# Optimization experiments

Hardware: AMD Instinct MI355X
Metric: run time of the kernel (lower is better)

## Reference

```python
import jax, jax.numpy as jnp
import numpy as np

INPUT_DIM = 256
HIDDEN_DIM = 512
BATCH = 64
SEQ = 512


def setup_inputs() -> dict:
    key = jax.random.key(0)
    k1, k2, k3, k4, k5 = jax.random.split(key, 5)
    s = 1.0 / np.sqrt(HIDDEN_DIM)
    x = jax.random.normal(k1, (BATCH, SEQ, INPUT_DIM), dtype=jnp.float32)
    # PyTorch GRU param layout: [3*H, in] with gate order (r, z, n)
    W_ih = jax.random.uniform(k2, (3 * HIDDEN_DIM, INPUT_DIM), minval=-s, maxval=s, dtype=jnp.float32)
    W_hh = jax.random.uniform(k3, (3 * HIDDEN_DIM, HIDDEN_DIM), minval=-s, maxval=s, dtype=jnp.float32)
    b_ih = jax.random.uniform(k4, (3 * HIDDEN_DIM,), minval=-s, maxval=s, dtype=jnp.float32)
    b_hh = jax.random.uniform(k5, (3 * HIDDEN_DIM,), minval=-s, maxval=s, dtype=jnp.float32)
    return {"x": x, "W_ih": W_ih, "W_hh": W_hh, "b_ih": b_ih, "b_hh": b_hh}


def _gru_last(x, W_ih, W_hh, b_ih, b_hh):
    B, T, _ = x.shape
    H = W_hh.shape[1]
    # Precompute input projections for all timesteps: [B, T, 3H]
    x_proj = jnp.einsum('bti,gi->btg', x, W_ih) + b_ih
    x_proj = jnp.swapaxes(x_proj, 0, 1)  # [T, B, 3H] for scan

    def step(h, xp):
        h_proj = h @ W_hh.T + b_hh  # [B, 3H]
        xr, xz, xn = jnp.split(xp, 3, axis=-1)
        hr, hz, hn = jnp.split(h_proj, 3, axis=-1)
        r = jax.nn.sigmoid(xr + hr)
        z = jax.nn.sigmoid(xz + hz)
        n = jnp.tanh(xn + r * hn)
        h_new = (1.0 - z) * n + z * h
        return h_new, None

    h0 = jnp.zeros((B, H), dtype=x.dtype)
    h_last, _ = jax.lax.scan(step, h0, x_proj)
    return h_last  # equals output[:, -1, :] for unidirectional single-layer GRU


def reference(x, W_ih, W_hh, b_ih, b_hh):
    return _gru_last(x, W_ih, W_hh, b_ih, b_hh)
```

## Files before the change

kernel.cpp:

```cpp
#include <hip/hip_runtime.h>
#include <hip/hip_bf16.h>


#define NB 64
#define NT 512
#define NI 256
#define NH 512

typedef __attribute__((ext_vector_type(8))) short bf16x8;
typedef __attribute__((ext_vector_type(4))) float f32x4;
typedef __attribute__((ext_vector_type(4))) int i32x4;

static __device__ __forceinline__ short f2b(float f) {
  unsigned u = __builtin_bit_cast(unsigned, f);
  unsigned r = (u + 0x7fffu + ((u >> 16) & 1u)) >> 16;
  return (short)r;
}
static __device__ __forceinline__ float sigm(float x) {
  return 1.0f / (1.0f + __expf(-x));
}
static __device__ __forceinline__ float tanh_f(float x) {
  return 1.0f - 2.0f / (__expf(2.0f * x) + 1.0f);
}

__global__ __launch_bounds__(256, 1)
void gru_persistent(const float* __restrict__ x,
                    const float* __restrict__ Wih,
                    const float* __restrict__ Whh,
                    const float* __restrict__ bih,
                    const float* __restrict__ bhh,
                    float* __restrict__ out,
                    unsigned char* __restrict__ ws) {
  const int wg   = blockIdx.x;
  const int tid  = threadIdx.x;
  const int wave = tid >> 6;
  const int lane = tid & 63;
  const int c    = lane & 15;
  const int q    = lane >> 4;

  int* slots = (int*)ws;
  int* tags  = (int*)(ws + 8192);
  unsigned short* hb0 = (unsigned short*)(ws + 16384);
  unsigned short* hb1 = (unsigned short*)(ws + 16384 + 65536);
  unsigned short* xb  = (unsigned short*)(ws + 16384 + 2 * 65536);

  __shared__ unsigned short trans[4][16][8];

  {
    const float4* x4 = (const float4*)x;
    const int total4 = NB * NT * NI / 4;
    const int nthr = NB * 256;
    for (int i = wg * 256 + tid; i < total4; i += nthr) {
      float4 v = x4[i];
      ushort4 o;
      o.x = (unsigned short)f2b(v.x);
      o.y = (unsigned short)f2b(v.y);
      o.z = (unsigned short)f2b(v.z);
      o.w = (unsigned short)f2b(v.w);
      ((ushort4*)xb)[i] = o;
    }
    ((unsigned int*)hb0)[wg * 256 + tid] = 0u;
    if (wg == 0) tags[tid] = 0;
  }

  bf16x8 wh[2][16];
  bf16x8 wi[2][8];
#pragma unroll
  for (int nt = 0; nt < 2; nt++) {
    int nl = nt * 16 + c;
    bool valid = nl < 24;
    int gate = nl >> 3;
    int jj = nl & 7;
    int grow = valid ? (gate * NH + wg * 8 + jj) : 0;
#pragma unroll
    for (int kk = 0; kk < 16; kk++) {
      const float* p = Whh + (size_t)grow * NH + kk * 32 + q * 8;
      bf16x8 f;
#pragma unroll
      for (int e = 0; e < 8; e++) f[e] = valid ? f2b(p[e]) : (short)0;
      wh[nt][kk] = f;
    }
#pragma unroll
    for (int kk = 0; kk < 8; kk++) {
      const float* p = Wih + (size_t)grow * NI + kk * 32 + q * 8;
      bf16x8 f;
#pragma unroll
      for (int e = 0; e < 8; e++) f[e] = valid ? f2b(p[e]) : (short)0;
      wi[nt][kk] = f;
    }
  }

  const int jcol = wg * 8 + (c & 7);
  const float bri = bih[jcol],          brh = bhh[jcol];
  const float bzi = bih[NH + jcol],     bzh = bhh[NH + jcol];
  const float bni = bih[2 * NH + jcol], bnh = bhh[2 * NH + jcol];

  float hold[4] = {0.f, 0.f, 0.f, 0.f};

  __syncthreads();
  if (tid == 0)
    __hip_atomic_store(&slots[wg * 32], 1, __ATOMIC_RELEASE,
                       __HIP_MEMORY_SCOPE_AGENT);
  if (wave == 0) {
    while (__hip_atomic_load(&slots[lane * 32], __ATOMIC_RELAXED,
                             __HIP_MEMORY_SCOPE_AGENT) < 1)
      __builtin_amdgcn_s_sleep(1);
  }
  __syncthreads();
  __threadfence();

  const int b0 = wave * 16 + c;
  int* mytags = tags + wave * 64;
  const int* tagp = mytags + lane;

  for (int t = 0; t < NT; t++) {
    const unsigned short* hcur = (t & 1) ? hb1 : hb0;
    unsigned short* hnext      = (t & 1) ? hb0 : hb1;

    f32x4 aX0 = {0.f, 0.f, 0.f, 0.f}, aX1 = {0.f, 0.f, 0.f, 0.f};
    f32x4 aH0 = {0.f, 0.f, 0.f, 0.f}, aH1 = {0.f, 0.f, 0.f, 0.f};

    const bf16x8* xr = (const bf16x8*)(xb + ((size_t)b0 * NT + t) * NI);

#pragma unroll
    for (int kk = 0; kk < 8; kk++) {
      bf16x8 a = xr[kk * 4 + q];
      aX0 = __builtin_amdgcn_mfma_f32_16x16x32_bf16(a, wi[0][kk], aX0, 0, 0, 0);
      aX1 = __builtin_amdgcn_mfma_f32_16x16x32_bf16(a, wi[1][kk], aX1, 0, 0, 0);
    }

    if (t > 0) {
      const int need = t + 1;
      while (true) {
        int v;
        asm volatile("global_load_dword %0, %1, off sc1"
                     : "=v"(v) : "v"(tagp));
        asm volatile("s_waitcnt vmcnt(0)" : "+v"(v)::"memory");
        if (__all(v >= need)) break;
      }
    }

    i32x4 hv[16];
    {
      const char* hb = (const char*)hcur;
#pragma unroll
      for (int kk = 0; kk < 16; kk++) {
        const void* ap = hb + (size_t)(((kk * 4 + q) * 64 + b0) << 4);
        asm volatile("global_load_dwordx4 %0, %1, off sc1"
                     : "=v"(hv[kk]) : "v"(ap));
      }
      asm volatile("s_waitcnt vmcnt(0)"
                   : "+v"(hv[0]), "+v"(hv[1]), "+v"(hv[2]), "+v"(hv[3]),
                     "+v"(hv[4]), "+v"(hv[5]), "+v"(hv[6]), "+v"(hv[7]),
                     "+v"(hv[8]), "+v"(hv[9]), "+v"(hv[10]), "+v"(hv[11]),
                     "+v"(hv[12]), "+v"(hv[13]), "+v"(hv[14]), "+v"(hv[15])
                   ::"memory");
    }

#pragma unroll
    for (int kk = 0; kk < 16; kk++) {
      bf16x8 a = __builtin_bit_cast(bf16x8, hv[kk]);
      aH0 = __builtin_amdgcn_mfma_f32_16x16x32_bf16(a, wh[0][kk], aH0, 0, 0, 0);
      aH1 = __builtin_amdgcn_mfma_f32_16x16x32_bf16(a, wh[1][kk], aH1, 0, 0, 0);
    }

#pragma unroll
    for (int r = 0; r < 4; r++) {
      float xz = __shfl_xor(aX0[r], 8, 64);
      float hz = __shfl_xor(aH0[r], 8, 64);
      float rr = sigm(aX0[r] + bri + aH0[r] + brh);
      float zz = sigm(xz + bzi + hz + bzh);
      float nn = tanh_f(aX1[r] + bni + rr * (aH1[r] + bnh));
      float hv2 = (1.0f - zz) * nn + zz * hold[r];
      hold[r] = hv2;
      if (c < 8) trans[wave][q * 4 + r][c] = (unsigned short)f2b(hv2);
    }

    if (t < NT - 1) {
      asm volatile("s_waitcnt lgkmcnt(0)" ::: "memory");
      if (lane < 16) {
        int b = wave * 16 + lane;
        const unsigned long long* tp =
            (const unsigned long long*)&trans[wave][lane][0];
        unsigned long long v0 = tp[0], v1 = tp[1];
        unsigned long long* dst =
            (unsigned long long*)(hnext + ((size_t)wg * 64 + b) * 8);
        __hip_atomic_store(dst, v0, __ATOMIC_RELAXED, __HIP_MEMORY_SCOPE_AGENT);
        __hip_atomic_store(dst + 1, v1, __ATOMIC_RELAXED,
                           __HIP_MEMORY_SCOPE_AGENT);
      }
      asm volatile("s_waitcnt vmcnt(0)" ::: "memory");
      if (lane == 0)
        __hip_atomic_store(&mytags[wg], t + 2, __ATOMIC_RELAXED,
                           __HIP_MEMORY_SCOPE_AGENT);
    }
  }

  if (c < 8) {
#pragma unroll
    for (int r = 0; r < 4; r++) {
      int b = wave * 16 + q * 4 + r;
      out[(size_t)b * NH + wg * 8 + c] = hold[r];
    }
  }
}

extern "C" void kernel_launch(void* const* d_in, const int* in_sizes, int n_in,
                              void* d_out, int out_size, void* d_ws, size_t ws_size,
                              hipStream_t stream) {
  const float* x   = (const float*)d_in[0];
  const float* Wih = (const float*)d_in[1];
  const float* Whh = (const float*)d_in[2];
  const float* bih = (const float*)d_in[3];
  const float* bhh = (const float*)d_in[4];
  float* out = (float*)d_out;
  hipLaunchKernelGGL(gru_persistent, dim3(NB), dim3(256), 0, stream,
                     x, Wih, Whh, bih, bhh, out, (unsigned char*)d_ws);
}
```

Baseline: 1.834 ms.

## Spread workgroups across XCDs and use non-coherent fast path with runtime coherence test

Launches 512 blocks so every eighth block (one per XCD stride) becomes a persistent worker while all blocks share the x-to-bf16 conversion. At startup the workers run a timestamp-based barrier and a store/invalidate/load coherence test. If it passes, the recurrent loop switches to plain stores and loads with buffer_inv instead of sc1 system-coherent accesses, which cuts the latency of each per-step h exchange. This depends on the assumption that co-located workers share a coherent L2. A timeout and a demotion flag fall back to the old sc1 path.

```diff
diff --git a/kernel.cpp b/kernel.cpp
--- a/kernel.cpp
+++ b/kernel.cpp
@@ -7,6 +7,17 @@
 #define NI 256
 #define NH 512
 
+#define OFF_FLAGS   0u
+#define OFF_TSB1    32768u
+#define OFF_TSB2    36864u
+#define OFF_TSB3    40960u
+#define OFF_DEMOTE  45056u
+#define OFF_TESTA   49152u
+#define OFF_TAGS    57344u
+#define OFF_HB0     65536u
+#define OFF_HB1     131072u
+#define OFF_XB      262144u
+
 typedef __attribute__((ext_vector_type(8))) short bf16x8;
 typedef __attribute__((ext_vector_type(4))) float f32x4;
 typedef __attribute__((ext_vector_type(4))) int i32x4;
@@ -23,72 +34,57 @@
   return 1.0f - 2.0f / (__expf(2.0f * x) + 1.0f);
 }
 
-__global__ __launch_bounds__(256, 1)
-void gru_persistent(const float* __restrict__ x,
-                    const float* __restrict__ Wih,
-                    const float* __restrict__ Whh,
-                    const float* __restrict__ bih,
-                    const float* __restrict__ bhh,
-                    float* __restrict__ out,
-                    unsigned char* __restrict__ ws) {
-  const int wg   = blockIdx.x;
-  const int tid  = threadIdx.x;
+static __device__ __forceinline__ void tsbar(unsigned char* base, int rank,
+                                             int tid, int wave, int lane,
+                                             unsigned long long t0) {
+  __syncthreads();
+  if (tid == 0)
+    __hip_atomic_store((unsigned long long*)(base + (size_t)rank * 64),
+                       __builtin_amdgcn_s_memrealtime(), __ATOMIC_RELEASE,
+                       __HIP_MEMORY_SCOPE_AGENT);
+  if (wave == 0) {
+    while (__hip_atomic_load(
+               (const unsigned long long*)(base + (size_t)lane * 64),
+               __ATOMIC_RELAXED, __HIP_MEMORY_SCOPE_AGENT) < t0)
+      __builtin_amdgcn_s_sleep(1);
+  }
+  __syncthreads();
+  __threadfence();
+}
+
+#define LOAD_ALL(FLAG)                                                        \
+  do {                                                                        \
+    const char* hbase_ = (const char*)hcur;                                   \
+    _Pragma("unroll") for (int kk2 = 0; kk2 < 16; kk2++) {                    \
+      const void* ap_ = hbase_ + (size_t)(((kk2 * 4 + q) * 64 + b0) << 4);    \
+      asm volatile("global_load_dwordx4 %0, %1, off " FLAG                    \
+                   : "=v"(hv[kk2]) : "v"(ap_));                               \
+    }                                                                         \
+  } while (0)
+
+#define WAIT_ALL()                                                            \
+  asm volatile("s_waitcnt vmcnt(0)"                                           \
+               : "+v"(hv[0]), "+v"(hv[1]), "+v"(hv[2]), "+v"(hv[3]),          \
+                 "+v"(hv[4]), "+v"(hv[5]), "+v"(hv[6]), "+v"(hv[7]),          \
+                 "+v"(hv[8]), "+v"(hv[9]), "+v"(hv[10]), "+v"(hv[11]),        \
+                 "+v"(hv[12]), "+v"(hv[13]), "+v"(hv[14]), "+v"(hv[15])       \
+               ::"memory")
+
+template <bool FAST>
+static __device__ __forceinline__ void worker_body(
+    int wg, int tid, const float* __restrict__ bih,
+    const float* __restrict__ bhh, float* __restrict__ out,
+    unsigned char* __restrict__ ws, const bf16x8 wh[2][16],
+    const bf16x8 wi[2][8], unsigned short (*trans)[16][8]) {
   const int wave = tid >> 6;
   const int lane = tid & 63;
   const int c    = lane & 15;
   const int q    = lane >> 4;
 
-  int* slots = (int*)ws;
-  int* tags  = (int*)(ws + 8192);
-  unsigned short* hb0 = (unsigned short*)(ws + 16384);
-  unsigned short* hb1 = (unsigned short*)(ws + 16384 + 65536);
-  unsigned short* xb  = (unsigned short*)(ws + 16384 + 2 * 65536);
-
-  __shared__ unsigned short trans[4][16][8];
-
-  {
-    const float4* x4 = (const float4*)x;
-    const int total4 = NB * NT * NI / 4;
-    const int nthr = NB * 256;
-    for (int i = wg * 256 + tid; i < total4; i += nthr) {
-      float4 v = x4[i];
-      ushort4 o;
-      o.x = (unsigned short)f2b(v.x);
-      o.y = (unsigned short)f2b(v.y);
-      o.z = (unsigned short)f2b(v.z);
-      o.w = (unsigned short)f2b(v.w);
-      ((ushort4*)xb)[i] = o;
-    }
-    ((unsigned int*)hb0)[wg * 256 + tid] = 0u;
-    if (wg == 0) tags[tid] = 0;
-  }
-
-  bf16x8 wh[2][16];
-  bf16x8 wi[2][8];
-#pragma unroll
-  for (int nt = 0; nt < 2; nt++) {
-    int nl = nt * 16 + c;
-    bool valid = nl < 24;
-    int gate = nl >> 3;
-    int jj = nl & 7;
-    int grow = valid ? (gate * NH + wg * 8 + jj) : 0;
-#pragma unroll
-    for (int kk = 0; kk < 16; kk++) {
-      const float* p = Whh + (size_t)grow * NH + kk * 32 + q * 8;
-      bf16x8 f;
-#pragma unroll
-      for (int e = 0; e < 8; e++) f[e] = valid ? f2b(p[e]) : (short)0;
-      wh[nt][kk] = f;
-    }
-#pragma unroll
-    for (int kk = 0; kk < 8; kk++) {
-      const float* p = Wih + (size_t)grow * NI + kk * 32 + q * 8;
-      bf16x8 f;
-#pragma unroll
-      for (int e = 0; e < 8; e++) f[e] = valid ? f2b(p[e]) : (short)0;
-      wi[nt][kk] = f;
-    }
-  }
+  int* tags = (int*)(ws + OFF_TAGS);
+  unsigned short* hb0 = (unsigned short*)(ws + OFF_HB0);
+  unsigned short* hb1 = (unsigned short*)(ws + OFF_HB1);
+  const unsigned short* xb = (const unsigned short*)(ws + OFF_XB);
 
   const int jcol = wg * 8 + (c & 7);
   const float bri = bih[jcol],          brh = bhh[jcol];
@@ -97,18 +93,6 @@
 
   float hold[4] = {0.f, 0.f, 0.f, 0.f};
 
-  __syncthreads();
-  if (tid == 0)
-    __hip_atomic_store(&slots[wg * 32], 1, __ATOMIC_RELEASE,
-                       __HIP_MEMORY_SCOPE_AGENT);
-  if (wave == 0) {
-    while (__hip_atomic_load(&slots[lane * 32], __ATOMIC_RELAXED,
-                             __HIP_MEMORY_SCOPE_AGENT) < 1)
-      __builtin_amdgcn_s_sleep(1);
-  }
-  __syncthreads();
-  __threadfence();
-
   const int b0 = wave * 16 + c;
   int* mytags = tags + wave * 64;
   const int* tagp = mytags + lane;
@@ -117,51 +101,50 @@
     const unsigned short* hcur = (t & 1) ? hb1 : hb0;
     unsigned short* hnext      = (t & 1) ? hb0 : hb1;
 
-    f32x4 aX0 = {0.f, 0.f, 0.f, 0.f}, aX1 = {0.f, 0.f, 0.f, 0.f};
-    f32x4 aH0 = {0.f, 0.f, 0.f, 0.f}, aH1 = {0.f, 0.f, 0.f, 0.f};
+    f32x4 aX0 = {0.f,0.f,0.f,0.f}, aX1 = {0.f,0.f,0.f,0.f};
+    f32x4 aH0 = {0.f,0.f,0.f,0.f}, aH1 = {0.f,0.f,0.f,0.f};
 
     const bf16x8* xr = (const bf16x8*)(xb + ((size_t)b0 * NT + t) * NI);
 
 #pragma unroll
     for (int kk = 0; kk < 8; kk++) {
       bf16x8 a = xr[kk * 4 + q];
-      aX0 = __builtin_amdgcn_mfma_f32_16x16x32_bf16(a, wi[0][kk], aX0, 0, 0, 0);
-      aX1 = __builtin_amdgcn_mfma_f32_16x16x32_bf16(a, wi[1][kk], aX1, 0, 0, 0);
+      aX0 = __builtin_amdgcn_mfma_f32_16x16x32_bf16(a, wi[0][kk], aX0, 0,0,0);
+      aX1 = __builtin_amdgcn_mfma_f32_16x16x32_bf16(a, wi[1][kk], aX1, 0,0,0);
     }
 
     if (t > 0) {
       const int need = t + 1;
-      while (true) {
-        int v;
-        asm volatile("global_load_dword %0, %1, off sc1"
-                     : "=v"(v) : "v"(tagp));
-        asm volatile("s_waitcnt vmcnt(0)" : "+v"(v)::"memory");
-        if (__all(v >= need)) break;
+      if (FAST) {
+        for (;;) {
+          asm volatile("buffer_inv sc0" ::: "memory");
+          int v;
+          asm volatile("global_load_dword %0, %1, off" : "=v"(v) : "v"(tagp));
+          asm volatile("s_waitcnt vmcnt(0)" : "+v"(v)::"memory");
+          if (__all(v >= need)) break;
+        }
+      } else {
+        for (;;) {
+          int v;
+          asm volatile("global_load_dword %0, %1, off sc1"
+                       : "=v"(v) : "v"(tagp));
+          asm volatile("s_waitcnt vmcnt(0)" : "+v"(v)::"memory");
+          if (__all(v >= need)) break;
+        }
       }
+    } else if (FAST) {
+      asm volatile("buffer_inv sc0" ::: "memory");
     }
 
     i32x4 hv[16];
-    {
-      const char* hb = (const char*)hcur;
-#pragma unroll
-      for (int kk = 0; kk < 16; kk++) {
-        const void* ap = hb + (size_t)(((kk * 4 + q) * 64 + b0) << 4);
-        asm volatile("global_load_dwordx4 %0, %1, off sc1"
-                     : "=v"(hv[kk]) : "v"(ap));
-      }
-      asm volatile("s_waitcnt vmcnt(0)"
-                   : "+v"(hv[0]), "+v"(hv[1]), "+v"(hv[2]), "+v"(hv[3]),
-                     "+v"(hv[4]), "+v"(hv[5]), "+v"(hv[6]), "+v"(hv[7]),
-                     "+v"(hv[8]), "+v"(hv[9]), "+v"(hv[10]), "+v"(hv[11]),
-                     "+v"(hv[12]), "+v"(hv[13]), "+v"(hv[14]), "+v"(hv[15])
-                   ::"memory");
-    }
+    if (FAST) LOAD_ALL(""); else LOAD_ALL("sc1");
+    WAIT_ALL();
 
 #pragma unroll
     for (int kk = 0; kk < 16; kk++) {
       bf16x8 a = __builtin_bit_cast(bf16x8, hv[kk]);
-      aH0 = __builtin_amdgcn_mfma_f32_16x16x32_bf16(a, wh[0][kk], aH0, 0, 0, 0);
-      aH1 = __builtin_amdgcn_mfma_f32_16x16x32_bf16(a, wh[1][kk], aH1, 0, 0, 0);
+      aH0 = __builtin_amdgcn_mfma_f32_16x16x32_bf16(a, wh[0][kk], aH0, 0,0,0);
+      aH1 = __builtin_amdgcn_mfma_f32_16x16x32_bf16(a, wh[1][kk], aH1, 0,0,0);
     }
 
 #pragma unroll
@@ -180,19 +163,26 @@
       asm volatile("s_waitcnt lgkmcnt(0)" ::: "memory");
       if (lane < 16) {
         int b = wave * 16 + lane;
-        const unsigned long long* tp =
-            (const unsigned long long*)&trans[wave][lane][0];
-        unsigned long long v0 = tp[0], v1 = tp[1];
-        unsigned long long* dst =
-            (unsigned long long*)(hnext + ((size_t)wg * 64 + b) * 8);
-        __hip_atomic_store(dst, v0, __ATOMIC_RELAXED, __HIP_MEMORY_SCOPE_AGENT);
-        __hip_atomic_store(dst + 1, v1, __ATOMIC_RELAXED,
-                           __HIP_MEMORY_SCOPE_AGENT);
+        i32x4 pk = *(const i32x4*)&trans[wave][lane][0];
+        void* dst = (char*)hnext + ((size_t)(wg * 64 + b) << 4);
+        if (FAST)
+          asm volatile("global_store_dwordx4 %0, %1, off"
+                       :: "v"(dst), "v"(pk) : "memory");
+        else
+          asm volatile("global_store_dwordx4 %0, %1, off sc1"
+                       :: "v"(dst), "v"(pk) : "memory");
       }
       asm volatile("s_waitcnt vmcnt(0)" ::: "memory");
-      if (lane == 0)
-        __hip_atomic_store(&mytags[wg], t + 2, __ATOMIC_RELAXED,
-                           __HIP_MEMORY_SCOPE_AGENT);
+      if (lane == 0) {
+        int* tp = &mytags[wg];
+        int tv = t + 2;
+        if (FAST)
+          asm volatile("global_store_dword %0, %1, off"
+                       :: "v"(tp), "v"(tv) : "memory");
+        else
+          __hip_atomic_store(tp, tv, __ATOMIC_RELAXED,
+                             __HIP_MEMORY_SCOPE_AGENT);
+      }
     }
   }
 
@@ -203,6 +193,146 @@
       out[(size_t)b * NH + wg * 8 + c] = hold[r];
     }
   }
+}
+
+__global__ __launch_bounds__(256, 2)
+void gru_persistent(const float* __restrict__ x,
+                    const float* __restrict__ Wih,
+                    const float* __restrict__ Whh,
+                    const float* __restrict__ bih,
+                    const float* __restrict__ bhh,
+                    float* __restrict__ out,
+                    unsigned char* __restrict__ ws) {
+  const int bid  = blockIdx.x;
+  const int tid  = threadIdx.x;
+  const int wave = tid >> 6;
+  const int lane = tid & 63;
+  const int c    = lane & 15;
+  const int q    = lane >> 4;
+
+  const unsigned long long t0 = __builtin_amdgcn_s_memrealtime();
+
+  unsigned long long* flags = (unsigned long long*)(ws + OFF_FLAGS);
+  int* tags = (int*)(ws + OFF_TAGS);
+  unsigned* hb0d = (unsigned*)(ws + OFF_HB0);
+  unsigned short* xb = (unsigned short*)(ws + OFF_XB);
+
+  __shared__ __align__(16) unsigned short trans[4][16][8];
+  __shared__ int s_bad;
+
+  const bool is_worker = (bid & 7) == 0;
+  const int rank = bid >> 3;
+
+  {
+    const float4* x4 = (const float4*)x;
+    const int total4 = NB * NT * NI / 4;
+    const int nthr = 512 * 256;
+    for (int i = bid * 256 + tid; i < total4; i += nthr) {
+      float4 v = x4[i];
+      ushort4 o;
+      o.x = (unsigned short)f2b(v.x);
+      o.y = (unsigned short)f2b(v.y);
+      o.z = (unsigned short)f2b(v.z);
+      o.w = (unsigned short)f2b(v.w);
+      ((ushort4*)xb)[i] = o;
+    }
+    if (is_worker) hb0d[rank * 256 + tid] = 0u;
+    if (bid == 0) tags[tid] = 0;
+  }
+
+  __syncthreads();
+  if (tid == 0)
+    __hip_atomic_store(&flags[bid * 8], __builtin_amdgcn_s_memrealtime(),
+                       __ATOMIC_RELEASE, __HIP_MEMORY_SCOPE_AGENT);
+  if (!is_worker) return;
+
+  bf16x8 wh[2][16];
+  bf16x8 wi[2][8];
+#pragma unroll
+  for (int nt = 0; nt < 2; nt++) {
+    int nl = nt * 16 + c;
+    bool valid = nl < 24;
+    int gate = nl >> 3;
+    int jj = nl & 7;
+    int grow = valid ? (gate * NH + rank * 8 + jj) : 0;
+#pragma unroll
+    for (int kk = 0; kk < 16; kk++) {
+      const float* p = Whh + (size_t)grow * NH + kk * 32 + q * 8;
+      bf16x8 f;
+#pragma unroll
+      for (int e = 0; e < 8; e++) f[e] = valid ? f2b(p[e]) : (short)0;
+      wh[nt][kk] = f;
+    }
+#pragma unroll
+    for (int kk = 0; kk < 8; kk++) {
+      const float* p = Wih + (size_t)grow * NI + kk * 32 + q * 8;
+      bf16x8 f;
+#pragma unroll
+      for (int e = 0; e < 8; e++) f[e] = valid ? f2b(p[e]) : (short)0;
+      wi[nt][kk] = f;
+    }
+  }
+
+  if (wave == 0) {
+#pragma unroll
+    for (int j = 0; j < 8; j++) {
+      const unsigned long long dl = t0 + 200000ull;
+      while (__hip_atomic_load(&flags[(lane * 8 + j) * 8], __ATOMIC_RELAXED,
+                               __HIP_MEMORY_SCOPE_AGENT) < t0) {
+        if (__builtin_amdgcn_s_memrealtime() > dl) break;
+        __builtin_amdgcn_s_sleep(1);
+      }
+    }
+  }
+  __syncthreads();
+  __threadfence();
+
+  if (tid == 0) s_bad = 0;
+  if (wave == 0) {
+    int v;
+    const void* p = ws + OFF_TESTA + (size_t)lane * 64;
+    asm volatile("global_load_dword %0, %1, off" : "=v"(v) : "v"(p));
+    asm volatile("s_waitcnt vmcnt(0)" : "+v"(v)::"memory");
+  }
+  tsbar(ws + OFF_TSB1, rank, tid, wave, lane, t0);
+  const unsigned ep = (unsigned)__hip_atomic_load(
+      (const unsigned long long*)(ws + OFF_TSB1), __ATOMIC_RELAXED,
+      __HIP_MEMORY_SCOPE_AGENT);
+  if (tid == 0) {
+    unsigned mg = (ep ^ 0x5EEDBEEFu) + (unsigned)rank * 2654435761u;
+    void* p = ws + OFF_TESTA + (size_t)rank * 64;
+    asm volatile("global_store_dword %0, %1, off" :: "v"(p), "v"(mg)
+                 : "memory");
+    asm volatile("s_waitcnt vmcnt(0)" ::: "memory");
+  }
+  tsbar(ws + OFF_TSB2, rank, tid, wave, lane, t0);
+  {
+    int bad = 0;
+    if (wave == 0) {
+      asm volatile("buffer_inv sc0" ::: "memory");
+      int v;
+      const void* p = ws + OFF_TESTA + (size_t)lane * 64;
+      asm volatile("global_load_dword %0, %1, off" : "=v"(v) : "v"(p));
+      asm volatile("s_waitcnt vmcnt(0)" : "+v"(v)::"memory");
+      unsigned want = (ep ^ 0x5EEDBEEFu) + (unsigned)lane * 2654435761u;
+      bad = (v != (int)want);
+    }
+    if (bad) s_bad = 1;
+    __syncthreads();
+    if (s_bad && tid == 0)
+      __hip_atomic_store((unsigned long long*)(ws + OFF_DEMOTE),
+                         __builtin_amdgcn_s_memrealtime(), __ATOMIC_RELEASE,
+                         __HIP_MEMORY_SCOPE_AGENT);
+  }
+  tsbar(ws + OFF_TSB3, rank, tid, wave, lane, t0);
+  const bool fast =
+      __hip_atomic_load((const unsigned long long*)(ws + OFF_DEMOTE),
+                        __ATOMIC_RELAXED, __HIP_MEMORY_SCOPE_AGENT) < t0;
+
+  if (fast)
+    worker_body<true>(rank, tid, bih, bhh, out, ws, wh, wi, trans);
+  else
+    worker_body<false>(rank, tid, bih, bhh, out, ws, wh, wi, trans);
 }
 
 extern "C" void kernel_launch(void* const* d_in, const int* in_sizes, int n_in,
@@ -214,6 +344,6 @@
   const float* bih = (const float*)d_in[3];
   const float* bhh = (const float*)d_in[4];
   float* out = (float*)d_out;
-  hipLaunchKernelGGL(gru_persistent, dim3(NB), dim3(256), 0, stream,
+  hipLaunchKernelGGL(gru_persistent, dim3(512), dim3(256), 0, stream,
                      x, Wih, Whh, bih, bhh, out, (unsigned char*)d_ws);
 }
```

Measured after the change: 3.999 ms. 118% more time.

## Probe L2 coherence at runtime and use non-sc1 loads with cache invalidate

Applied to the files above, without the earlier changes.

Launches 512 blocks and keeps only every eighth one, so the 64 working groups are likely spread across separate XCDs. At startup it runs a coherence test through plain stores and loads plus buffer_inv. If every group sees every other group's writes, the recurrence loop uses ordinary global loads and stores with a per-step L1 invalidate instead of sc1-scoped accesses. Barriers now compare timestamps so they work without resetting the workspace. This adds startup barriers, and relying on an empirical coherence test is fragile.

```diff
diff --git a/kernel.cpp b/kernel.cpp
--- a/kernel.cpp
+++ b/kernel.cpp
@@ -7,6 +7,14 @@
 #define NI 256
 #define NH 512
 
+#define OFF_TSB    0u
+#define OFF_DEMOTE 32768u
+#define OFF_TESTA  36864u
+#define OFF_TAGS   40960u
+#define OFF_HB0    65536u
+#define OFF_HB1    131072u
+#define OFF_XB     262144u
+
 typedef __attribute__((ext_vector_type(8))) short bf16x8;
 typedef __attribute__((ext_vector_type(4))) float f32x4;
 typedef __attribute__((ext_vector_type(4))) int i32x4;
@@ -23,7 +31,98 @@
   return 1.0f - 2.0f / (__expf(2.0f * x) + 1.0f);
 }
 
-__global__ __launch_bounds__(256, 1)
+static __device__ __forceinline__ void tsbar(unsigned char* ws, int idx,
+                                             int rank, int tid, int wave,
+                                             int lane,
+                                             unsigned long long t0) {
+  unsigned long long* base =
+      (unsigned long long*)(ws + OFF_TSB + (unsigned)idx * 4096u);
+  __syncthreads();
+  if (tid == 0)
+    __hip_atomic_store(&base[rank * 8], __builtin_amdgcn_s_memrealtime(),
+                       __ATOMIC_RELEASE, __HIP_MEMORY_SCOPE_AGENT);
+  if (wave == 0) {
+    while (__hip_atomic_load(&base[lane * 8], __ATOMIC_RELAXED,
+                             __HIP_MEMORY_SCOPE_AGENT) < t0)
+      __builtin_amdgcn_s_sleep(1);
+  }
+  __syncthreads();
+  __threadfence();
+}
+
+#define TLOOP(LDSUF, STSUF, FASTINV)                                          \
+  for (int t = 0; t < NT; t++) {                                              \
+    const unsigned short* hcur = (t & 1) ? hb1 : hb0;                         \
+    unsigned short* hnext      = (t & 1) ? hb0 : hb1;                         \
+    f32x4 aX0 = {0.f,0.f,0.f,0.f}, aX1 = {0.f,0.f,0.f,0.f};                   \
+    f32x4 aH0 = {0.f,0.f,0.f,0.f}, aH1 = {0.f,0.f,0.f,0.f};                   \
+    const bf16x8* xr = (const bf16x8*)(xb + ((size_t)b0 * NT + t) * NI);      \
+    _Pragma("unroll") for (int kk = 0; kk < 8; kk++) {                        \
+      bf16x8 a = xr[kk * 4 + q];                                              \
+      aX0 = __builtin_amdgcn_mfma_f32_16x16x32_bf16(a, wi[0][kk], aX0,0,0,0); \
+      aX1 = __builtin_amdgcn_mfma_f32_16x16x32_bf16(a, wi[1][kk], aX1,0,0,0); \
+    }                                                                         \
+    if (t > 0) {                                                              \
+      const int need = t + 1;                                                 \
+      for (;;) {                                                              \
+        if (FASTINV) asm volatile("buffer_inv sc0" ::: "memory");             \
+        int v;                                                                \
+        asm volatile("global_load_dword %0, %1, off" LDSUF                    \
+                     : "=v"(v) : "v"(tagp));                                  \
+        asm volatile("s_waitcnt vmcnt(0)" : "+v"(v) :: "memory");             \
+        if (__all(v >= need)) break;                                          \
+      }                                                                       \
+    } else if (FASTINV) {                                                     \
+      asm volatile("buffer_inv sc0" ::: "memory");                            \
+    }                                                                         \
+    i32x4 hv[16];                                                             \
+    _Pragma("unroll") for (int kk2 = 0; kk2 < 16; kk2++) {                    \
+      const void* ap_ =                                                       \
+          (const char*)hcur + (size_t)(((kk2 * 4 + q) * 64 + b0) << 4);       \
+      asm volatile("global_load_dwordx4 %0, %1, off" LDSUF                    \
+                   : "=v"(hv[kk2]) : "v"(ap_));                               \
+    }                                                                         \
+    asm volatile("s_waitcnt vmcnt(0)"                                         \
+                 : "+v"(hv[0]), "+v"(hv[1]), "+v"(hv[2]), "+v"(hv[3]),        \
+                   "+v"(hv[4]), "+v"(hv[5]), "+v"(hv[6]), "+v"(hv[7]),        \
+                   "+v"(hv[8]), "+v"(hv[9]), "+v"(hv[10]), "+v"(hv[11]),      \
+                   "+v"(hv[12]), "+v"(hv[13]), "+v"(hv[14]), "+v"(hv[15])     \
+                 ::"memory");                                                 \
+    _Pragma("unroll") for (int kk = 0; kk < 16; kk++) {                       \
+      bf16x8 a = __builtin_bit_cast(bf16x8, hv[kk]);                          \
+      aH0 = __builtin_amdgcn_mfma_f32_16x16x32_bf16(a, wh[0][kk], aH0,0,0,0); \
+      aH1 = __builtin_amdgcn_mfma_f32_16x16x32_bf16(a, wh[1][kk], aH1,0,0,0); \
+    }                                                                         \
+    _Pragma("unroll") for (int r = 0; r < 4; r++) {                           \
+      float xz = __shfl_xor(aX0[r], 8, 64);                                   \
+      float hz = __shfl_xor(aH0[r], 8, 64);                                   \
+      float rr = sigm(aX0[r] + bri + aH0[r] + brh);                           \
+      float zz = sigm(xz + bzi + hz + bzh);                                   \
+      float nn = tanh_f(aX1[r] + bni + rr * (aH1[r] + bnh));                  \
+      float hv2 = (1.0f - zz) * nn + zz * hold[r];                            \
+      hold[r] = hv2;                                                          \
+      if (c < 8) trans[wave][q * 4 + r][c] = (unsigned short)f2b(hv2);        \
+    }                                                                         \
+    if (t < NT - 1) {                                                         \
+      asm volatile("s_waitcnt lgkmcnt(0)" ::: "memory");                      \
+      if (lane < 16) {                                                        \
+        int b = wave * 16 + lane;                                             \
+        i32x4 pk = *(const i32x4*)&trans[wave][lane][0];                      \
+        void* dst = (char*)hnext + ((size_t)(wg * 64 + b) << 4);              \
+        asm volatile("global_store_dwordx4 %0, %1, off" STSUF                 \
+                     :: "v"(dst), "v"(pk) : "memory");                        \
+      }                                                                       \
+      asm volatile("s_waitcnt vmcnt(0)" ::: "memory");                        \
+      if (lane == 0) {                                                        \
+        int* tp = &mytags[wg];                                                \
+        int tv = t + 2;                                                       \
+        asm volatile("global_store_dword %0, %1, off" STSUF                   \
+                     :: "v"(tp), "v"(tv) : "memory");                         \
+      }                                                                       \
+    }                                                                         \
+  }
+
+__global__ __launch_bounds__(256, 2)
 void gru_persistent(const float* __restrict__ x,
                     const float* __restrict__ Wih,
                     const float* __restrict__ Whh,
@@ -31,25 +130,29 @@
                     const float* __restrict__ bhh,
                     float* __restrict__ out,
                     unsigned char* __restrict__ ws) {
-  const int wg   = blockIdx.x;
+  const int bid = blockIdx.x;
+  if (bid & 7) return;
+  const int wg  = bid >> 3;
   const int tid  = threadIdx.x;
   const int wave = tid >> 6;
   const int lane = tid & 63;
   const int c    = lane & 15;
   const int q    = lane >> 4;
 
-  int* slots = (int*)ws;
-  int* tags  = (int*)(ws + 8192);
-  unsigned short* hb0 = (unsigned short*)(ws + 16384);
-  unsigned short* hb1 = (unsigned short*)(ws + 16384 + 65536);
-  unsigned short* xb  = (unsigned short*)(ws + 16384 + 2 * 65536);
-
-  __shared__ unsigned short trans[4][16][8];
+  const unsigned long long t0 = __builtin_amdgcn_s_memrealtime();
+
+  int* tags = (int*)(ws + OFF_TAGS);
+  unsigned short* hb0 = (unsigned short*)(ws + OFF_HB0);
+  unsigned short* hb1 = (unsigned short*)(ws + OFF_HB1);
+  unsigned short* xb  = (unsigned short*)(ws + OFF_XB);
+
+  __shared__ __align__(16) unsigned short trans[4][16][8];
+  __shared__ int s_bad;
 
   {
     const float4* x4 = (const float4*)x;
     const int total4 = NB * NT * NI / 4;
-    const int nthr = NB * 256;
+    const int nthr = 64 * 256;
     for (int i = wg * 256 + tid; i < total4; i += nthr) {
       float4 v = x4[i];
       ushort4 o;
@@ -59,7 +162,7 @@
       o.w = (unsigned short)f2b(v.w);
       ((ushort4*)xb)[i] = o;
     }
-    ((unsigned int*)hb0)[wg * 256 + tid] = 0u;
+    ((unsigned*)hb0)[wg * 256 + tid] = 0u;
     if (wg == 0) tags[tid] = 0;
   }
 
@@ -97,103 +200,63 @@
 
   float hold[4] = {0.f, 0.f, 0.f, 0.f};
 
+  tsbar(ws, 0, wg, tid, wave, lane, t0);
+
+  if (tid == 0) s_bad = 0;
   __syncthreads();
-  if (tid == 0)
-    __hip_atomic_store(&slots[wg * 32], 1, __ATOMIC_RELEASE,
-                       __HIP_MEMORY_SCOPE_AGENT);
-  if (wave == 0) {
-    while (__hip_atomic_load(&slots[lane * 32], __ATOMIC_RELAXED,
-                             __HIP_MEMORY_SCOPE_AGENT) < 1)
-      __builtin_amdgcn_s_sleep(1);
-  }
-  __syncthreads();
-  __threadfence();
+#pragma unroll 1
+  for (int rnd = 0; rnd < 2; rnd++) {
+    if (wave == 0) {
+      int v;
+      const void* p = ws + OFF_TESTA + (size_t)lane * 64;
+      asm volatile("global_load_dword %0, %1, off" : "=v"(v) : "v"(p));
+      asm volatile("s_waitcnt vmcnt(0)" : "+v"(v)::"memory");
+    }
+    tsbar(ws, 1 + rnd * 3, wg, tid, wave, lane, t0);
+    const unsigned ep = (unsigned)__hip_atomic_load(
+        (const unsigned long long*)(ws + OFF_TSB + (1 + rnd * 3) * 4096u),
+        __ATOMIC_RELAXED, __HIP_MEMORY_SCOPE_AGENT);
+    if (tid == 0) {
+      unsigned mg = (ep ^ 0x5EEDBEEFu) + (unsigned)wg * 2654435761u;
+      void* p = ws + OFF_TESTA + (size_t)wg * 64;
+      asm volatile("global_store_dword %0, %1, off" :: "v"(p), "v"(mg)
+                   : "memory");
+      asm volatile("s_waitcnt vmcnt(0)" ::: "memory");
+    }
+    tsbar(ws, 2 + rnd * 3, wg, tid, wave, lane, t0);
+    {
+      int bad = 0;
+      if (wave == 0) {
+        asm volatile("buffer_inv sc0" ::: "memory");
+        int v;
+        const void* p = ws + OFF_TESTA + (size_t)lane * 64;
+        asm volatile("global_load_dword %0, %1, off" : "=v"(v) : "v"(p));
+        asm volatile("s_waitcnt vmcnt(0)" : "+v"(v)::"memory");
+        unsigned want = (ep ^ 0x5EEDBEEFu) + (unsigned)lane * 2654435761u;
+        bad = (v != (int)want);
+      }
+      if (bad) s_bad = 1;
+      __syncthreads();
+      if (s_bad && tid == 0)
+        __hip_atomic_store((unsigned long long*)(ws + OFF_DEMOTE),
+                           __builtin_amdgcn_s_memrealtime(),
+                           __ATOMIC_RELEASE, __HIP_MEMORY_SCOPE_AGENT);
+      __syncthreads();
+    }
+    tsbar(ws, 3 + rnd * 3, wg, tid, wave, lane, t0);
+  }
+  const bool fast =
+      __hip_atomic_load((const unsigned long long*)(ws + OFF_DEMOTE),
+                        __ATOMIC_RELAXED, __HIP_MEMORY_SCOPE_AGENT) < t0;
 
   const int b0 = wave * 16 + c;
   int* mytags = tags + wave * 64;
   const int* tagp = mytags + lane;
 
-  for (int t = 0; t < NT; t++) {
-    const unsigned short* hcur = (t & 1) ? hb1 : hb0;
-    unsigned short* hnext      = (t & 1) ? hb0 : hb1;
-
-    f32x4 aX0 = {0.f, 0.f, 0.f, 0.f}, aX1 = {0.f, 0.f, 0.f, 0.f};
-    f32x4 aH0 = {0.f, 0.f, 0.f, 0.f}, aH1 = {0.f, 0.f, 0.f, 0.f};
-
-    const bf16x8* xr = (const bf16x8*)(xb + ((size_t)b0 * NT + t) * NI);
-
-#pragma unroll
-    for (int kk = 0; kk < 8; kk++) {
-      bf16x8 a = xr[kk * 4 + q];
-      aX0 = __builtin_amdgcn_mfma_f32_16x16x32_bf16(a, wi[0][kk], aX0, 0, 0, 0);
-      aX1 = __builtin_amdgcn_mfma_f32_16x16x32_bf16(a, wi[1][kk], aX1, 0, 0, 0);
-    }
-
-    if (t > 0) {
-      const int need = t + 1;
-      while (true) {
-        int v;
-        asm volatile("global_load_dword %0, %1, off sc1"
-                     : "=v"(v) : "v"(tagp));
-        asm volatile("s_waitcnt vmcnt(0)" : "+v"(v)::"memory");
-        if (__all(v >= need)) break;
-      }
-    }
-
-    i32x4 hv[16];
-    {
-      const char* hb = (const char*)hcur;
-#pragma unroll
-      for (int kk = 0; kk < 16; kk++) {
-        const void* ap = hb + (size_t)(((kk * 4 + q) * 64 + b0) << 4);
-        asm volatile("global_load_dwordx4 %0, %1, off sc1"
-                     : "=v"(hv[kk]) : "v"(ap));
-      }
-      asm volatile("s_waitcnt vmcnt(0)"
-                   : "+v"(hv[0]), "+v"(hv[1]), "+v"(hv[2]), "+v"(hv[3]),
-                     "+v"(hv[4]), "+v"(hv[5]), "+v"(hv[6]), "+v"(hv[7]),
-                     "+v"(hv[8]), "+v"(hv[9]), "+v"(hv[10]), "+v"(hv[11]),
-                     "+v"(hv[12]), "+v"(hv[13]), "+v"(hv[14]), "+v"(hv[15])
-                   ::"memory");
-    }
-
-#pragma unroll
-    for (int kk = 0; kk < 16; kk++) {
-      bf16x8 a = __builtin_bit_cast(bf16x8, hv[kk]);
-      aH0 = __builtin_amdgcn_mfma_f32_16x16x32_bf16(a, wh[0][kk], aH0, 0, 0, 0);
-      aH1 = __builtin_amdgcn_mfma_f32_16x16x32_bf16(a, wh[1][kk], aH1, 0, 0, 0);
-    }
-
-#pragma unroll
-    for (int r = 0; r < 4; r++) {
-      float xz = __shfl_xor(aX0[r], 8, 64);
-      float hz = __shfl_xor(aH0[r], 8, 64);
-      float rr = sigm(aX0[r] + bri + aH0[r] + brh);
-      float zz = sigm(xz + bzi + hz + bzh);
-      float nn = tanh_f(aX1[r] + bni + rr * (aH1[r] + bnh));
-      float hv2 = (1.0f - zz) * nn + zz * hold[r];
-      hold[r] = hv2;
-      if (c < 8) trans[wave][q * 4 + r][c] = (unsigned short)f2b(hv2);
-    }
-
-    if (t < NT - 1) {
-      asm volatile("s_waitcnt lgkmcnt(0)" ::: "memory");
-      if (lane < 16) {
-        int b = wave * 16 + lane;
-        const unsigned long long* tp =
-            (const unsigned long long*)&trans[wave][lane][0];
-        unsigned long long v0 = tp[0], v1 = tp[1];
-        unsigned long long* dst =
-            (unsigned long long*)(hnext + ((size_t)wg * 64 + b) * 8);
-        __hip_atomic_store(dst, v0, __ATOMIC_RELAXED, __HIP_MEMORY_SCOPE_AGENT);
-        __hip_atomic_store(dst + 1, v1, __ATOMIC_RELAXED,
-                           __HIP_MEMORY_SCOPE_AGENT);
-      }
-      asm volatile("s_waitcnt vmcnt(0)" ::: "memory");
-      if (lane == 0)
-        __hip_atomic_store(&mytags[wg], t + 2, __ATOMIC_RELAXED,
-                           __HIP_MEMORY_SCOPE_AGENT);
-    }
+  if (fast) {
+    TLOOP("", "", 1)
+  } else {
+    TLOOP(" sc1", " sc1", 0)
   }
 
   if (c < 8) {
@@ -214,6 +277,6 @@
   const float* bih = (const float*)d_in[3];
   const float* bhh = (const float*)d_in[4];
   float* out = (float*)d_out;
-  hipLaunchKernelGGL(gru_persistent, dim3(NB), dim3(256), 0, stream,
+  hipLaunchKernelGGL(gru_persistent, dim3(512), dim3(256), 0, stream,
                      x, Wih, Whh, bih, bhh, out, (unsigned char*)d_ws);
 }
```

Measured after the change: 4.139 ms. 2.26x slower.

## Replicate step tags, rotate h load order, timestamp start barrier, vector h store

Applied to the files above, without the earlier changes.

Each wave now writes its progress tag to four replicated tag arrays, and workgroups poll different replicas, which spreads polling traffic across more cache lines. The hidden-state loads are issued in a per-workgroup rotated order so that workgroups hit different addresses at the same moment. The start barrier compares against realtime timestamps instead of a constant, so the workspace needs no reset between launches. The h store becomes a single 16-byte vector store, in exchange for four tag stores per step instead of one.

```diff
diff --git a/kernel.cpp b/kernel.cpp
--- a/kernel.cpp
+++ b/kernel.cpp
@@ -22,6 +22,17 @@
 static __device__ __forceinline__ float tanh_f(float x) {
   return 1.0f - 2.0f / (__expf(2.0f * x) + 1.0f);
 }
+
+#define ISSUE16(R)                                                            \
+  do {                                                                        \
+    _Pragma("unroll") for (int i_ = 0; i_ < 16; i_++) {                       \
+      const int kk2 = (i_ + (R)) & 15;                                        \
+      const void* ap_ =                                                       \
+          (const char*)hcur + (size_t)(((kk2 * 4 + q) * 64 + b0) << 4);       \
+      asm volatile("global_load_dwordx4 %0, %1, off sc1"                      \
+                   : "=v"(hv[kk2]) : "v"(ap_));                               \
+    }                                                                         \
+  } while (0)
 
 __global__ __launch_bounds__(256, 1)
 void gru_persistent(const float* __restrict__ x,
@@ -38,13 +49,15 @@
   const int c    = lane & 15;
   const int q    = lane >> 4;
 
-  int* slots = (int*)ws;
-  int* tags  = (int*)(ws + 8192);
+  const unsigned long long t0 = __builtin_amdgcn_s_memrealtime();
+
+  unsigned long long* flags = (unsigned long long*)ws;
+  int* tags = (int*)(ws + 8192);
   unsigned short* hb0 = (unsigned short*)(ws + 16384);
   unsigned short* hb1 = (unsigned short*)(ws + 16384 + 65536);
   unsigned short* xb  = (unsigned short*)(ws + 16384 + 2 * 65536);
 
-  __shared__ unsigned short trans[4][16][8];
+  __shared__ __align__(16) unsigned short trans[4][16][8];
 
   {
     const float4* x4 = (const float4*)x;
@@ -60,7 +73,10 @@
       ((ushort4*)xb)[i] = o;
     }
     ((unsigned int*)hb0)[wg * 256 + tid] = 0u;
-    if (wg == 0) tags[tid] = 0;
+    if (wg == 0) {
+#pragma unroll
+      for (int r2 = 0; r2 < 4; r2++) tags[r2 * 256 + tid] = 0;
+    }
   }
 
   bf16x8 wh[2][16];
@@ -99,19 +115,19 @@
 
   __syncthreads();
   if (tid == 0)
-    __hip_atomic_store(&slots[wg * 32], 1, __ATOMIC_RELEASE,
-                       __HIP_MEMORY_SCOPE_AGENT);
+    __hip_atomic_store(&flags[wg * 8], __builtin_amdgcn_s_memrealtime(),
+                       __ATOMIC_RELEASE, __HIP_MEMORY_SCOPE_AGENT);
   if (wave == 0) {
-    while (__hip_atomic_load(&slots[lane * 32], __ATOMIC_RELAXED,
-                             __HIP_MEMORY_SCOPE_AGENT) < 1)
+    while (__hip_atomic_load(&flags[lane * 8], __ATOMIC_RELAXED,
+                             __HIP_MEMORY_SCOPE_AGENT) < t0)
       __builtin_amdgcn_s_sleep(1);
   }
   __syncthreads();
   __threadfence();
 
   const int b0 = wave * 16 + c;
-  int* mytags = tags + wave * 64;
-  const int* tagp = mytags + lane;
+  const int rot = wg & 7;
+  const int* tagp = tags + (wg & 3) * 256 + wave * 64 + lane;
 
   for (int t = 0; t < NT; t++) {
     const unsigned short* hcur = (t & 1) ? hb1 : hb0;
@@ -131,7 +147,7 @@
 
     if (t > 0) {
       const int need = t + 1;
-      while (true) {
+      for (;;) {
         int v;
         asm volatile("global_load_dword %0, %1, off sc1"
                      : "=v"(v) : "v"(tagp));
@@ -141,21 +157,20 @@
     }
 
     i32x4 hv[16];
-    {
-      const char* hb = (const char*)hcur;
-#pragma unroll
-      for (int kk = 0; kk < 16; kk++) {
-        const void* ap = hb + (size_t)(((kk * 4 + q) * 64 + b0) << 4);
-        asm volatile("global_load_dwordx4 %0, %1, off sc1"
-                     : "=v"(hv[kk]) : "v"(ap));
-      }
-      asm volatile("s_waitcnt vmcnt(0)"
-                   : "+v"(hv[0]), "+v"(hv[1]), "+v"(hv[2]), "+v"(hv[3]),
-                     "+v"(hv[4]), "+v"(hv[5]), "+v"(hv[6]), "+v"(hv[7]),
-                     "+v"(hv[8]), "+v"(hv[9]), "+v"(hv[10]), "+v"(hv[11]),
-                     "+v"(hv[12]), "+v"(hv[13]), "+v"(hv[14]), "+v"(hv[15])
-                   ::"memory");
-    }
+    if      (rot == 0) ISSUE16(0);
+    else if (rot == 1) ISSUE16(2);
+    else if (rot == 2) ISSUE16(4);
+    else if (rot == 3) ISSUE16(6);
+    else if (rot == 4) ISSUE16(8);
+    else if (rot == 5) ISSUE16(10);
+    else if (rot == 6) ISSUE16(12);
+    else               ISSUE16(14);
+    asm volatile("s_waitcnt vmcnt(0)"
+                 : "+v"(hv[0]), "+v"(hv[1]), "+v"(hv[2]), "+v"(hv[3]),
+                   "+v"(hv[4]), "+v"(hv[5]), "+v"(hv[6]), "+v"(hv[7]),
+                   "+v"(hv[8]), "+v"(hv[9]), "+v"(hv[10]), "+v"(hv[11]),
+                   "+v"(hv[12]), "+v"(hv[13]), "+v"(hv[14]), "+v"(hv[15])
+                 ::"memory");
 
 #pragma unroll
     for (int kk = 0; kk < 16; kk++) {
@@ -180,19 +195,18 @@
       asm volatile("s_waitcnt lgkmcnt(0)" ::: "memory");
       if (lane < 16) {
         int b = wave * 16 + lane;
-        const unsigned long long* tp =
-            (const unsigned long long*)&trans[wave][lane][0];
-        unsigned long long v0 = tp[0], v1 = tp[1];
-        unsigned long long* dst =
-            (unsigned long long*)(hnext + ((size_t)wg * 64 + b) * 8);
-        __hip_atomic_store(dst, v0, __ATOMIC_RELAXED, __HIP_MEMORY_SCOPE_AGENT);
-        __hip_atomic_store(dst + 1, v1, __ATOMIC_RELAXED,
-                           __HIP_MEMORY_SCOPE_AGENT);
+        i32x4 pk = *(const i32x4*)&trans[wave][lane][0];
+        void* dst = (char*)hnext + ((size_t)(wg * 64 + b) << 4);
+        asm volatile("global_store_dwordx4 %0, %1, off sc1"
+                     :: "v"(dst), "v"(pk) : "memory");
       }
       asm volatile("s_waitcnt vmcnt(0)" ::: "memory");
-      if (lane == 0)
-        __hip_atomic_store(&mytags[wg], t + 2, __ATOMIC_RELAXED,
-                           __HIP_MEMORY_SCOPE_AGENT);
+      if (lane == 0) {
+#pragma unroll
+        for (int r2 = 0; r2 < 4; r2++)
+          __hip_atomic_store(&tags[r2 * 256 + wave * 64 + wg], t + 2,
+                             __ATOMIC_RELAXED, __HIP_MEMORY_SCOPE_AGENT);
+      }
     }
   }
 
```

Result: slower. 1.917 ms (+4.5%).
